# Kernel tuning notes

Measured on AMD Instinct MI355X. Metric: run time of the kernel, lower is better.

The kernel has to match this reference:

```python
import jax, jax.numpy as jnp
import numpy as np

NUM_HEADS = 8
HEAD_DIM = 64  # embed_dim 512 / 8 heads


def setup_inputs() -> dict:
    key = jax.random.key(0)
    k1, k2, k3 = jax.random.split(key, 3)
    B, S, D = 2, 4096, 512
    # xavier-uniform-ish scales for faithfulness to init (values don't affect math)
    x = jax.random.normal(k1, (B, S, D), dtype=jnp.float32)
    qkv_w = jax.random.normal(k2, (3 * D, D), dtype=jnp.float32) * (1.0 / np.sqrt(D))
    qkv_b = jnp.zeros((3 * D,), dtype=jnp.float32)
    o_w = jax.random.normal(k3, (D, D), dtype=jnp.float32) * (1.0 / np.sqrt(D))
    o_b = jnp.zeros((D,), dtype=jnp.float32)
    return {"x": x, "qkv_w": qkv_w, "qkv_b": qkv_b, "o_w": o_w, "o_b": o_b}


def reference(x, qkv_w, qkv_b, o_w, o_b):
    B, S, D = x.shape
    H, hd = NUM_HEADS, HEAD_DIM
    # qkv projection: torch Linear is x @ W^T + b
    qkv = jnp.einsum('bsd,ed->bse', x, qkv_w) + qkv_b        # [B, S, 3D]
    qkv = qkv.reshape(B, S, H, 3 * hd).transpose(0, 2, 1, 3)  # [B, H, S, 3hd]
    q, k, v = jnp.split(qkv, 3, axis=-1)                      # each [B, H, S, hd]
    scale = 1.0 / jnp.sqrt(jnp.float32(hd))
    logits = jnp.einsum('bhqd,bhkd->bhqk', q, k) * scale      # [B, H, S, S]
    attn = jax.nn.softmax(logits, axis=-1)
    vals = jnp.einsum('bhqk,bhkd->bhqd', attn, v)             # [B, H, S, hd]
    vals = vals.transpose(0, 2, 1, 3).reshape(B, S, D)        # [B, S, D]
    o = jnp.einsum('bsd,ed->bse', vals, o_w) + o_b            # [B, S, D]
    return o
```

## Files before the change

### kernel.cpp

```cpp
#include <hip/hip_runtime.h>
#include <hip/hip_bf16.h>


typedef __attribute__((ext_vector_type(8)))  __bf16 bf16x8;
typedef __attribute__((ext_vector_type(2)))  __bf16 bf16x2;
typedef __attribute__((ext_vector_type(4))) float  f32x4;
typedef __attribute__((ext_vector_type(16))) float  f32x16;

__device__ __forceinline__ unsigned cvtpk(float a, float b) {
    bf16x2 t; t.x = (__bf16)a; t.y = (__bf16)b;
    union { bf16x2 v; unsigned u; } u; u.v = t; return u.u;
}
#if __has_builtin(__builtin_amdgcn_exp2f)
__device__ __forceinline__ float fexp2(float x) { return __builtin_amdgcn_exp2f(x); }
#else
__device__ __forceinline__ float fexp2(float x) { return exp2f(x); }
#endif
__device__ __forceinline__ void gload16(const unsigned short* g, unsigned short* l) {
    __builtin_amdgcn_global_load_lds(
        (const __attribute__((address_space(1))) void*)g,
        (__attribute__((address_space(3))) void*)l, 16, 0, 0);
}

__device__ __forceinline__ int swz(int row, int col) {
    return row * 64 + (col ^ ((row & 7) << 3));
}

__global__ __launch_bounds__(256) void qkv_qk_gemm(
    const float* __restrict__ X, const float* __restrict__ W,
    const float* __restrict__ bias,
    unsigned short* __restrict__ Qb, unsigned short* __restrict__ Kb)
{
    __shared__ __attribute__((aligned(16))) unsigned short SH[128 * 144];
    unsigned short* As = &SH[0];
    unsigned short* Bs = &SH[8192];
    const int tid = threadIdx.x;
    const int wid = tid >> 6, lane = tid & 63;
    const int hi = lane >> 4, lo = lane & 15;
    const int wm = wid >> 1, wn = wid & 1;
    const int m0 = blockIdx.x * 128;
    const int by3 = blockIdx.y & 3, tt = blockIdx.y >> 2;
    const float QSCL = 0.125f * 1.44269504088896f;
    const float sc = (tt == 0) ? QSCL : 1.0f;

    f32x4 acc[4][4] = {};

    for (int k0 = 0; k0 < 512; k0 += 64) {
        __syncthreads();
        #pragma unroll
        for (int i = 0; i < 8; ++i) {
            const int c = i * 256 + tid;
            const int row = c >> 4, kc = (c & 15) << 2;
            const float4 va = *(const float4*)(X + (size_t)(m0 + row) * 512 + k0 + kc);
            uint2 pa; pa.x = cvtpk(va.x, va.y); pa.y = cvtpk(va.z, va.w);
            *(uint2*)&As[swz(row, kc)] = pa;
            const int nW = (by3 * 2 + (row >> 6)) * 192 + tt * 64 + (row & 63);
            const float4 vb = *(const float4*)(W + (size_t)nW * 512 + k0 + kc);
            uint2 pb; pb.x = cvtpk(vb.x, vb.y); pb.y = cvtpk(vb.z, vb.w);
            *(uint2*)&Bs[swz(row, kc)] = pb;
        }
        __syncthreads();
        #pragma unroll
        for (int ks = 0; ks < 2; ++ks) {
            bf16x8 af[4], bfr[4];
            #pragma unroll
            for (int mi = 0; mi < 4; ++mi)
                af[mi] = *(const bf16x8*)&As[swz(wm * 64 + mi * 16 + lo, ks * 32 + hi * 8)];
            #pragma unroll
            for (int ni = 0; ni < 4; ++ni)
                bfr[ni] = *(const bf16x8*)&Bs[swz(wn * 64 + ni * 16 + lo, ks * 32 + hi * 8)];
            #pragma unroll
            for (int mi = 0; mi < 4; ++mi)
                #pragma unroll
                for (int ni = 0; ni < 4; ++ni)
                    acc[mi][ni] = __builtin_amdgcn_mfma_f32_16x16x32_bf16(
                        bfr[ni], af[mi], acc[mi][ni], 0, 0, 0);
        }
    }
    __syncthreads();

    {
        #pragma unroll
        for (int ni = 0; ni < 4; ++ni) {
            const int hq = by3 * 2 + wn;
            const float4 bv4 = *(const float4*)&bias[hq * 192 + tt * 64 + ni * 16 + hi * 4];
            #pragma unroll
            for (int mi = 0; mi < 4; ++mi) {
                const int srow_ = wm * 64 + mi * 16 + lo;
                uint2 w;
                w.x = cvtpk((acc[mi][ni][0] + bv4.x) * sc, (acc[mi][ni][1] + bv4.y) * sc);
                w.y = cvtpk((acc[mi][ni][2] + bv4.z) * sc, (acc[mi][ni][3] + bv4.w) * sc);
                *(uint2*)&SH[srow_ * 144 + wn * 72 + ni * 16 + hi * 4] = w;
            }
        }
    }
    __syncthreads();

    const int b = m0 >> 12, sb = m0 & 4095;
    unsigned short* dst = tt ? Kb : Qb;
    #pragma unroll
    for (int c = 0; c < 2; ++c) {
        const int h = by3 * 2 + c;
        #pragma unroll
        for (int qq = 0; qq < 4; ++qq) {
            const int slot = qq * 256 + tid;
            const int row = slot >> 3, g = slot & 7;
            const uint4 v = *(const uint4*)&SH[row * 144 + c * 72 + g * 8];
            *(uint4*)(dst + (((size_t)(b * 8 + h)) * 4096 + sb + row) * 64 + g * 8) = v;
        }
    }
}

__global__ __launch_bounds__(256) void qkv_v_gemm(
    const float* __restrict__ X, const float* __restrict__ W,
    const float* __restrict__ bias, unsigned short* __restrict__ Vtg)
{
    __shared__ __attribute__((aligned(16))) unsigned short SH[128 * 144];
    unsigned short* As = &SH[0];
    unsigned short* Bs = &SH[8192];
    const int tid = threadIdx.x;
    const int wid = tid >> 6, lane = tid & 63;
    const int hi = lane >> 4, lo = lane & 15;
    const int wm = wid >> 1, wn = wid & 1;
    const int m0 = blockIdx.x * 128;
    const int by = blockIdx.y;

    f32x4 acc[4][4] = {};

    for (int k0 = 0; k0 < 512; k0 += 64) {
        __syncthreads();
        #pragma unroll
        for (int i = 0; i < 8; ++i) {
            const int c = i * 256 + tid;
            const int row = c >> 4, kc = (c & 15) << 2;
            const float4 va = *(const float4*)(X + (size_t)(m0 + row) * 512 + k0 + kc);
            uint2 pa; pa.x = cvtpk(va.x, va.y); pa.y = cvtpk(va.z, va.w);
            *(uint2*)&As[swz(row, kc)] = pa;
            const int nW = (by * 2 + (row >> 6)) * 192 + 128 + (row & 63);
            const float4 vb = *(const float4*)(W + (size_t)nW * 512 + k0 + kc);
            uint2 pb; pb.x = cvtpk(vb.x, vb.y); pb.y = cvtpk(vb.z, vb.w);
            *(uint2*)&Bs[swz(row, kc)] = pb;
        }
        __syncthreads();
        #pragma unroll
        for (int ks = 0; ks < 2; ++ks) {
            bf16x8 af[4], bfr[4];
            #pragma unroll
            for (int mi = 0; mi < 4; ++mi)
                af[mi] = *(const bf16x8*)&As[swz(wm * 64 + mi * 16 + lo, ks * 32 + hi * 8)];
            #pragma unroll
            for (int ni = 0; ni < 4; ++ni)
                bfr[ni] = *(const bf16x8*)&Bs[swz(wn * 64 + ni * 16 + lo, ks * 32 + hi * 8)];
            #pragma unroll
            for (int mi = 0; mi < 4; ++mi)
                #pragma unroll
                for (int ni = 0; ni < 4; ++ni)
                    acc[mi][ni] = __builtin_amdgcn_mfma_f32_16x16x32_bf16(
                        af[mi], bfr[ni], acc[mi][ni], 0, 0, 0);
        }
    }
    __syncthreads();

    #pragma unroll
    for (int ni = 0; ni < 4; ++ni) {
        const int d = ni * 16 + lo;
        const float bv = bias[(by * 2 + wn) * 192 + 128 + d];
        #pragma unroll
        for (int mi = 0; mi < 4; ++mi) {
            const int ml = wm * 64 + mi * 16 + hi * 4;
            uint2 w;
            w.x = cvtpk(acc[mi][ni][0] + bv, acc[mi][ni][1] + bv);
            w.y = cvtpk(acc[mi][ni][2] + bv, acc[mi][ni][3] + bv);
            *(uint2*)&SH[wn * 8704 + d * 136 + ml] = w;
        }
    }
    __syncthreads();

    const int b = m0 >> 12, sb = m0 & 4095;
    #pragma unroll
    for (int qq = 0; qq < 8; ++qq) {
        const int slot = qq * 256 + tid;
        const int c = slot >> 10, d = (slot >> 4) & 63, mb = slot & 15;
        const int src = c * 8704 + d * 136 + 16 * (mb >> 1) + 4 * (mb & 1);
        const uint2 a  = *(const uint2*)&SH[src];
        const uint2 bb = *(const uint2*)&SH[src + 8];
        uint4 w; w.x = a.x; w.y = a.y; w.z = bb.x; w.w = bb.y;
        const int h = by * 2 + c;
        *(uint4*)(Vtg + ((size_t)((b * 8 + h) * 64 + d)) * 4096 + sb + 8 * mb) = w;
    }
}

__global__ __launch_bounds__(512, 2) void attn_fwd(
    const unsigned short* __restrict__ Qb,
    const unsigned short* __restrict__ Kb,
    const unsigned short* __restrict__ Vtg,
    unsigned short* __restrict__ Ob)
{
    __shared__ __attribute__((aligned(16))) unsigned short smem[2][4][2][4096];

    const int tid = threadIdx.x;
    const int wid = tid >> 6, lane = tid & 63;
    const int l31 = lane & 31, hl = lane >> 5;
    const int n_ = blockIdx.x;
    const int bh = (n_ & 7) * 2 + ((n_ >> 3) & 1);
    const int qb = n_ >> 4;
    const int b = bh >> 3, h = bh & 7;
    const int q0 = qb * 256 + wid * 32;
    const size_t kbase = (size_t)bh * 4096 * 64;
    const size_t vbase = (size_t)bh * 64 * 4096;

    const int srow = tid >> 3;
    const int sg = (tid & 7) ^ (srow & 7);
    const unsigned short* kS = Kb + kbase + (size_t)srow * 64 + sg * 8;
    const unsigned short* vS = Vtg + vbase + (size_t)srow * 4096 + sg * 8;

    bf16x8 qf[4];
    #pragma unroll
    for (int dk = 0; dk < 4; ++dk)
        qf[dk] = *(const bf16x8*)(Qb + kbase + (size_t)(q0 + l31) * 64 + dk * 16 + hl * 8);

    f32x16 o0 = {}, o1 = {};
    float l_run = 0.0f;

    const int s7 = l31 & 7;
    const int baseA = l31 * 64, baseB = (32 + l31) * 64;
    const int ldst = tid * 8;

    #pragma unroll
    for (int i = 0; i < 4; ++i) {
        gload16(kS + (size_t)i * 4096, &smem[0][i][0][ldst]);
        gload16(vS + (size_t)i * 64,   &smem[0][i][1][ldst]);
    }
    asm volatile("s_waitcnt vmcnt(0)" ::: "memory");
    __builtin_amdgcn_s_barrier();
    __builtin_amdgcn_sched_barrier(0);

    for (int g = 0; g < 16; ++g) {
        const int cur = g & 1;
        if (g < 15) {
            #pragma unroll
            for (int i = 0; i < 4; ++i) {
                const size_t T = 4 * (g + 1) + i;
                gload16(kS + T * 4096, &smem[cur ^ 1][i][0][ldst]);
                gload16(vS + T * 64,   &smem[cur ^ 1][i][1][ldst]);
            }
        }
        #pragma unroll
        for (int ti = 0; ti < 4; ++ti) {
            const unsigned short* KT = &smem[cur][ti][0][0];
            const unsigned short* VT = &smem[cur][ti][1][0];

            f32x16 s0 = {}, s1 = {};
            __builtin_amdgcn_s_setprio(1);
            #pragma unroll
            for (int dk = 0; dk < 4; ++dk) {
                const int gk = dk * 2 + hl;
                const bf16x8 kA = *(const bf16x8*)(KT + baseA + 8 * (gk ^ s7));
                const bf16x8 kB = *(const bf16x8*)(KT + baseB + 8 * (gk ^ s7));
                s0 = __builtin_amdgcn_mfma_f32_32x32x16_bf16(kA, qf[dk], s0, 0, 0, 0);
                s1 = __builtin_amdgcn_mfma_f32_32x32x16_bf16(kB, qf[dk], s1, 0, 0, 0);
            }
            __builtin_amdgcn_s_setprio(0);

            #pragma unroll
            for (int i = 0; i < 16; ++i) {
                s0[i] = fexp2(s0[i]);
                s1[i] = fexp2(s1[i]);
            }
            float lsA = 0.f, lsB = 0.f, lsC = 0.f, lsD = 0.f;
            #pragma unroll
            for (int i = 0; i < 4; ++i) {
                lsA += s0[i];      lsB += s0[i + 4];
                lsA += s0[i + 8];  lsB += s0[i + 12];
                lsC += s1[i];      lsD += s1[i + 4];
                lsC += s1[i + 8];  lsD += s1[i + 12];
            }
            l_run += (lsA + lsB) + (lsC + lsD);

            union U8 { unsigned u[4]; bf16x8 v; };
            U8 p0, p1, p2, p3;
            #pragma unroll
            for (int i = 0; i < 4; ++i) {
                p0.u[i] = cvtpk(s0[2 * i],     s0[2 * i + 1]);
                p1.u[i] = cvtpk(s0[2 * i + 8], s0[2 * i + 9]);
                p2.u[i] = cvtpk(s1[2 * i],     s1[2 * i + 1]);
                p3.u[i] = cvtpk(s1[2 * i + 8], s1[2 * i + 9]);
            }
            const bf16x8 pf[4] = { p0.v, p1.v, p2.v, p3.v };

            __builtin_amdgcn_s_setprio(1);
            #pragma unroll
            for (int ks = 0; ks < 4; ++ks) {
                const int gv = ((2 * ks + hl) ^ s7) << 3;
                const bf16x8 va = *(const bf16x8*)(VT + baseA + gv);
                const bf16x8 vb = *(const bf16x8*)(VT + baseB + gv);
                o0 = __builtin_amdgcn_mfma_f32_32x32x16_bf16(va, pf[ks], o0, 0, 0, 0);
                o1 = __builtin_amdgcn_mfma_f32_32x32x16_bf16(vb, pf[ks], o1, 0, 0, 0);
            }
            __builtin_amdgcn_s_setprio(0);
        }
        asm volatile("s_waitcnt vmcnt(0)" ::: "memory");
        __builtin_amdgcn_s_barrier();
        __builtin_amdgcn_sched_barrier(0);
    }

    l_run += __shfl_xor(l_run, 32);
    unsigned short* Ew = &smem[0][0][0][0] + wid * 2048;
    const int prow = l31 * 64;
    const float inv = 1.0f / l_run;
    #pragma unroll
    for (int u = 0; u < 4; ++u) {
        uint2 w0, w1;
        w0.x = cvtpk(o0[4 * u] * inv, o0[4 * u + 1] * inv);
        w0.y = cvtpk(o0[4 * u + 2] * inv, o0[4 * u + 3] * inv);
        *(uint2*)&Ew[prow + ((u ^ s7) << 3) + (hl << 2)] = w0;
        w1.x = cvtpk(o1[4 * u] * inv, o1[4 * u + 1] * inv);
        w1.y = cvtpk(o1[4 * u + 2] * inv, o1[4 * u + 3] * inv);
        *(uint2*)&Ew[prow + (((4 + u) ^ s7) << 3) + (hl << 2)] = w1;
    }
    asm volatile("s_waitcnt lgkmcnt(0)" ::: "memory");
    __builtin_amdgcn_sched_barrier(0);
    #pragma unroll
    for (int rr = 0; rr < 4; ++rr) {
        const int qrow = (lane >> 3) + rr * 8;
        const int gphys = (lane & 7) ^ (qrow & 7);
        const uint4 v = *(const uint4*)&Ew[qrow * 64 + gphys * 8];
        *(uint4*)(Ob + ((size_t)b * 4096 + q0 + qrow) * 512 + h * 64 + (lane & 7) * 8) = v;
    }
}

__global__ __launch_bounds__(256) void oproj_gemm(
    const unsigned short* __restrict__ A, const float* __restrict__ W,
    const float* __restrict__ bias, float* __restrict__ C)
{
    __shared__ __attribute__((aligned(16))) unsigned short As[128 * 64];
    __shared__ __attribute__((aligned(16))) unsigned short Bs[128 * 64];
    const int tid = threadIdx.x;
    const int wid = tid >> 6, lane = tid & 63;
    const int hi = lane >> 4, lo = lane & 15;
    const int wm = wid >> 1, wn = wid & 1;
    const int m0 = blockIdx.x * 128, n0 = blockIdx.y * 128;

    f32x4 acc[4][4] = {};
    for (int k0 = 0; k0 < 512; k0 += 64) {
        __syncthreads();
        #pragma unroll
        for (int i = 0; i < 4; ++i) {
            const int c = i * 256 + tid;
            const int row = c >> 3, kc = (c & 7) << 3;
            *(uint4*)&As[swz(row, kc)] =
                *(const uint4*)(A + (size_t)(m0 + row) * 512 + k0 + kc);
        }
        #pragma unroll
        for (int i = 0; i < 8; ++i) {
            const int c = i * 256 + tid;
            const int row = c >> 4, kc = (c & 15) << 2;
            const float4 vb = *(const float4*)(W + (size_t)(n0 + row) * 512 + k0 + kc);
            uint2 pb; pb.x = cvtpk(vb.x, vb.y); pb.y = cvtpk(vb.z, vb.w);
            *(uint2*)&Bs[swz(row, kc)] = pb;
        }
        __syncthreads();
        #pragma unroll
        for (int ks = 0; ks < 2; ++ks) {
            bf16x8 af[4], bfr[4];
            #pragma unroll
            for (int mi = 0; mi < 4; ++mi)
                af[mi] = *(const bf16x8*)&As[swz(wm * 64 + mi * 16 + lo, ks * 32 + hi * 8)];
            #pragma unroll
            for (int ni = 0; ni < 4; ++ni)
                bfr[ni] = *(const bf16x8*)&Bs[swz(wn * 64 + ni * 16 + lo, ks * 32 + hi * 8)];
            #pragma unroll
            for (int mi = 0; mi < 4; ++mi)
                #pragma unroll
                for (int ni = 0; ni < 4; ++ni)
                    acc[mi][ni] = __builtin_amdgcn_mfma_f32_16x16x32_bf16(
                        af[mi], bfr[ni], acc[mi][ni], 0, 0, 0);
        }
    }

    #pragma unroll
    for (int mi = 0; mi < 4; ++mi) {
        #pragma unroll
        for (int ni = 0; ni < 4; ++ni) {
            const int n = n0 + wn * 64 + ni * 16 + lo;
            const float bv = bias[n];
            #pragma unroll
            for (int j = 0; j < 4; ++j) {
                const int m = m0 + wm * 64 + mi * 16 + hi * 4 + j;
                C[(size_t)m * 512 + n] = acc[mi][ni][j] + bv;
            }
        }
    }
}

extern "C" void kernel_launch(void* const* d_in, const int* in_sizes, int n_in,
                              void* d_out, int out_size, void* d_ws, size_t ws_size,
                              hipStream_t stream) {
    const float* x     = (const float*)d_in[0];
    const float* qkv_w = (const float*)d_in[1];
    const float* qkv_b = (const float*)d_in[2];
    const float* o_w   = (const float*)d_in[3];
    const float* o_b   = (const float*)d_in[4];
    float* out = (float*)d_out;

    const size_t NELEM = (size_t)2 * 8 * 4096 * 64;
    unsigned short* Qb  = (unsigned short*)d_ws;
    unsigned short* Kb  = Qb + NELEM;
    unsigned short* Vtg = Kb + NELEM;
    unsigned short* Ob  = Vtg + NELEM;

    qkv_qk_gemm<<<dim3(64, 8), 256, 0, stream>>>(x, qkv_w, qkv_b, Qb, Kb);
    qkv_v_gemm<<<dim3(64, 4), 256, 0, stream>>>(x, qkv_w, qkv_b, Vtg);
    attn_fwd<<<dim3(256), 512, 0, stream>>>(Qb, Kb, Vtg, Ob);
    oproj_gemm<<<dim3(64, 4), 256, 0, stream>>>(Ob, o_w, o_b, out);
}
```

Baseline: 124.2 us.

## Merge QK and V projection kernels; vectorize row-sum and unroll attention loop

The separate Q/K and V projection GEMMs become one launch with a 64x12 grid, where blocks with y>=8 take the V path. This removes a kernel launch and lets all projection blocks run in one wave. In the attention kernel, the softmax row-sum moves after the PV MFMAs and is accumulated with packed 2-wide float adds. The main loop also gets `#pragma unroll 2`. The unroll and the reordering may raise register pressure.

```diff
diff --git a/kernel.cpp b/kernel.cpp
--- a/kernel.cpp
+++ b/kernel.cpp
@@ -4,6 +4,7 @@
 
 typedef __attribute__((ext_vector_type(8)))  __bf16 bf16x8;
 typedef __attribute__((ext_vector_type(2)))  __bf16 bf16x2;
+typedef __attribute__((ext_vector_type(2))) float  f32x2;
 typedef __attribute__((ext_vector_type(4))) float  f32x4;
 typedef __attribute__((ext_vector_type(16))) float  f32x16;
 
@@ -26,10 +27,11 @@
     return row * 64 + (col ^ ((row & 7) << 3));
 }
 
-__global__ __launch_bounds__(256) void qkv_qk_gemm(
+__global__ __launch_bounds__(256) void qkv_gemm(
     const float* __restrict__ X, const float* __restrict__ W,
     const float* __restrict__ bias,
-    unsigned short* __restrict__ Qb, unsigned short* __restrict__ Kb)
+    unsigned short* __restrict__ Qb, unsigned short* __restrict__ Kb,
+    unsigned short* __restrict__ Vtg)
 {
     __shared__ __attribute__((aligned(16))) unsigned short SH[128 * 144];
     unsigned short* As = &SH[0];
@@ -39,47 +41,50 @@
     const int hi = lane >> 4, lo = lane & 15;
     const int wm = wid >> 1, wn = wid & 1;
     const int m0 = blockIdx.x * 128;
-    const int by3 = blockIdx.y & 3, tt = blockIdx.y >> 2;
-    const float QSCL = 0.125f * 1.44269504088896f;
-    const float sc = (tt == 0) ? QSCL : 1.0f;
+    const bool isV = (blockIdx.y >= 8);
+    const int b = m0 >> 12, sb = m0 & 4095;
 
     f32x4 acc[4][4] = {};
 
-    for (int k0 = 0; k0 < 512; k0 += 64) {
-        __syncthreads();
-        #pragma unroll
-        for (int i = 0; i < 8; ++i) {
-            const int c = i * 256 + tid;
-            const int row = c >> 4, kc = (c & 15) << 2;
-            const float4 va = *(const float4*)(X + (size_t)(m0 + row) * 512 + k0 + kc);
-            uint2 pa; pa.x = cvtpk(va.x, va.y); pa.y = cvtpk(va.z, va.w);
-            *(uint2*)&As[swz(row, kc)] = pa;
-            const int nW = (by3 * 2 + (row >> 6)) * 192 + tt * 64 + (row & 63);
-            const float4 vb = *(const float4*)(W + (size_t)nW * 512 + k0 + kc);
-            uint2 pb; pb.x = cvtpk(vb.x, vb.y); pb.y = cvtpk(vb.z, vb.w);
-            *(uint2*)&Bs[swz(row, kc)] = pb;
-        }
-        __syncthreads();
-        #pragma unroll
-        for (int ks = 0; ks < 2; ++ks) {
-            bf16x8 af[4], bfr[4];
-            #pragma unroll
-            for (int mi = 0; mi < 4; ++mi)
-                af[mi] = *(const bf16x8*)&As[swz(wm * 64 + mi * 16 + lo, ks * 32 + hi * 8)];
-            #pragma unroll
-            for (int ni = 0; ni < 4; ++ni)
-                bfr[ni] = *(const bf16x8*)&Bs[swz(wn * 64 + ni * 16 + lo, ks * 32 + hi * 8)];
-            #pragma unroll
-            for (int mi = 0; mi < 4; ++mi)
+    if (!isV) {
+        const int by3 = blockIdx.y & 3, tt = blockIdx.y >> 2;
+        const float QSCL = 0.125f * 1.44269504088896f;
+        const float sc = (tt == 0) ? QSCL : 1.0f;
+
+        for (int k0 = 0; k0 < 512; k0 += 64) {
+            __syncthreads();
+            #pragma unroll
+            for (int i = 0; i < 8; ++i) {
+                const int c = i * 256 + tid;
+                const int row = c >> 4, kc = (c & 15) << 2;
+                const float4 va = *(const float4*)(X + (size_t)(m0 + row) * 512 + k0 + kc);
+                uint2 pa; pa.x = cvtpk(va.x, va.y); pa.y = cvtpk(va.z, va.w);
+                *(uint2*)&As[swz(row, kc)] = pa;
+                const int nW = (by3 * 2 + (row >> 6)) * 192 + tt * 64 + (row & 63);
+                const float4 vb = *(const float4*)(W + (size_t)nW * 512 + k0 + kc);
+                uint2 pb; pb.x = cvtpk(vb.x, vb.y); pb.y = cvtpk(vb.z, vb.w);
+                *(uint2*)&Bs[swz(row, kc)] = pb;
+            }
+            __syncthreads();
+            #pragma unroll
+            for (int ks = 0; ks < 2; ++ks) {
+                bf16x8 af[4], bfr[4];
+                #pragma unroll
+                for (int mi = 0; mi < 4; ++mi)
+                    af[mi] = *(const bf16x8*)&As[swz(wm * 64 + mi * 16 + lo, ks * 32 + hi * 8)];
                 #pragma unroll
                 for (int ni = 0; ni < 4; ++ni)
-                    acc[mi][ni] = __builtin_amdgcn_mfma_f32_16x16x32_bf16(
-                        bfr[ni], af[mi], acc[mi][ni], 0, 0, 0);
-        }
-    }
-    __syncthreads();
-
-    {
+                    bfr[ni] = *(const bf16x8*)&Bs[swz(wn * 64 + ni * 16 + lo, ks * 32 + hi * 8)];
+                #pragma unroll
+                for (int mi = 0; mi < 4; ++mi)
+                    #pragma unroll
+                    for (int ni = 0; ni < 4; ++ni)
+                        acc[mi][ni] = __builtin_amdgcn_mfma_f32_16x16x32_bf16(
+                            bfr[ni], af[mi], acc[mi][ni], 0, 0, 0);
+            }
+        }
+        __syncthreads();
+
         #pragma unroll
         for (int ni = 0; ni < 4; ++ni) {
             const int hq = by3 * 2 + wn;
@@ -93,100 +98,83 @@
                 *(uint2*)&SH[srow_ * 144 + wn * 72 + ni * 16 + hi * 4] = w;
             }
         }
-    }
-    __syncthreads();
-
-    const int b = m0 >> 12, sb = m0 & 4095;
-    unsigned short* dst = tt ? Kb : Qb;
-    #pragma unroll
-    for (int c = 0; c < 2; ++c) {
-        const int h = by3 * 2 + c;
-        #pragma unroll
-        for (int qq = 0; qq < 4; ++qq) {
+        __syncthreads();
+
+        unsigned short* dst = tt ? Kb : Qb;
+        #pragma unroll
+        for (int c = 0; c < 2; ++c) {
+            const int h = by3 * 2 + c;
+            #pragma unroll
+            for (int qq = 0; qq < 4; ++qq) {
+                const int slot = qq * 256 + tid;
+                const int row = slot >> 3, g = slot & 7;
+                const uint4 v = *(const uint4*)&SH[row * 144 + c * 72 + g * 8];
+                *(uint4*)(dst + (((size_t)(b * 8 + h)) * 4096 + sb + row) * 64 + g * 8) = v;
+            }
+        }
+    } else {
+        const int by = blockIdx.y - 8;
+
+        for (int k0 = 0; k0 < 512; k0 += 64) {
+            __syncthreads();
+            #pragma unroll
+            for (int i = 0; i < 8; ++i) {
+                const int c = i * 256 + tid;
+                const int row = c >> 4, kc = (c & 15) << 2;
+                const float4 va = *(const float4*)(X + (size_t)(m0 + row) * 512 + k0 + kc);
+                uint2 pa; pa.x = cvtpk(va.x, va.y); pa.y = cvtpk(va.z, va.w);
+                *(uint2*)&As[swz(row, kc)] = pa;
+                const int nW = (by * 2 + (row >> 6)) * 192 + 128 + (row & 63);
+                const float4 vb = *(const float4*)(W + (size_t)nW * 512 + k0 + kc);
+                uint2 pb; pb.x = cvtpk(vb.x, vb.y); pb.y = cvtpk(vb.z, vb.w);
+                *(uint2*)&Bs[swz(row, kc)] = pb;
+            }
+            __syncthreads();
+            #pragma unroll
+            for (int ks = 0; ks < 2; ++ks) {
+                bf16x8 af[4], bfr[4];
+                #pragma unroll
+                for (int mi = 0; mi < 4; ++mi)
+                    af[mi] = *(const bf16x8*)&As[swz(wm * 64 + mi * 16 + lo, ks * 32 + hi * 8)];
+                #pragma unroll
+                for (int ni = 0; ni < 4; ++ni)
+                    bfr[ni] = *(const bf16x8*)&Bs[swz(wn * 64 + ni * 16 + lo, ks * 32 + hi * 8)];
+                #pragma unroll
+                for (int mi = 0; mi < 4; ++mi)
+                    #pragma unroll
+                    for (int ni = 0; ni < 4; ++ni)
+                        acc[mi][ni] = __builtin_amdgcn_mfma_f32_16x16x32_bf16(
+                            af[mi], bfr[ni], acc[mi][ni], 0, 0, 0);
+            }
+        }
+        __syncthreads();
+
+        #pragma unroll
+        for (int ni = 0; ni < 4; ++ni) {
+            const int d = ni * 16 + lo;
+            const float bv = bias[(by * 2 + wn) * 192 + 128 + d];
+            #pragma unroll
+            for (int mi = 0; mi < 4; ++mi) {
+                const int ml = wm * 64 + mi * 16 + hi * 4;
+                uint2 w;
+                w.x = cvtpk(acc[mi][ni][0] + bv, acc[mi][ni][1] + bv);
+                w.y = cvtpk(acc[mi][ni][2] + bv, acc[mi][ni][3] + bv);
+                *(uint2*)&SH[wn * 8704 + d * 136 + ml] = w;
+            }
+        }
+        __syncthreads();
+
+        #pragma unroll
+        for (int qq = 0; qq < 8; ++qq) {
             const int slot = qq * 256 + tid;
-            const int row = slot >> 3, g = slot & 7;
-            const uint4 v = *(const uint4*)&SH[row * 144 + c * 72 + g * 8];
-            *(uint4*)(dst + (((size_t)(b * 8 + h)) * 4096 + sb + row) * 64 + g * 8) = v;
-        }
-    }
-}
-
-__global__ __launch_bounds__(256) void qkv_v_gemm(
-    const float* __restrict__ X, const float* __restrict__ W,
-    const float* __restrict__ bias, unsigned short* __restrict__ Vtg)
-{
-    __shared__ __attribute__((aligned(16))) unsigned short SH[128 * 144];
-    unsigned short* As = &SH[0];
-    unsigned short* Bs = &SH[8192];
-    const int tid = threadIdx.x;
-    const int wid = tid >> 6, lane = tid & 63;
-    const int hi = lane >> 4, lo = lane & 15;
-    const int wm = wid >> 1, wn = wid & 1;
-    const int m0 = blockIdx.x * 128;
-    const int by = blockIdx.y;
-
-    f32x4 acc[4][4] = {};
-
-    for (int k0 = 0; k0 < 512; k0 += 64) {
-        __syncthreads();
-        #pragma unroll
-        for (int i = 0; i < 8; ++i) {
-            const int c = i * 256 + tid;
-            const int row = c >> 4, kc = (c & 15) << 2;
-            const float4 va = *(const float4*)(X + (size_t)(m0 + row) * 512 + k0 + kc);
-            uint2 pa; pa.x = cvtpk(va.x, va.y); pa.y = cvtpk(va.z, va.w);
-            *(uint2*)&As[swz(row, kc)] = pa;
-            const int nW = (by * 2 + (row >> 6)) * 192 + 128 + (row & 63);
-            const float4 vb = *(const float4*)(W + (size_t)nW * 512 + k0 + kc);
-            uint2 pb; pb.x = cvtpk(vb.x, vb.y); pb.y = cvtpk(vb.z, vb.w);
-            *(uint2*)&Bs[swz(row, kc)] = pb;
-        }
-        __syncthreads();
-        #pragma unroll
-        for (int ks = 0; ks < 2; ++ks) {
-            bf16x8 af[4], bfr[4];
-            #pragma unroll
-            for (int mi = 0; mi < 4; ++mi)
-                af[mi] = *(const bf16x8*)&As[swz(wm * 64 + mi * 16 + lo, ks * 32 + hi * 8)];
-            #pragma unroll
-            for (int ni = 0; ni < 4; ++ni)
-                bfr[ni] = *(const bf16x8*)&Bs[swz(wn * 64 + ni * 16 + lo, ks * 32 + hi * 8)];
-            #pragma unroll
-            for (int mi = 0; mi < 4; ++mi)
-                #pragma unroll
-                for (int ni = 0; ni < 4; ++ni)
-                    acc[mi][ni] = __builtin_amdgcn_mfma_f32_16x16x32_bf16(
-                        af[mi], bfr[ni], acc[mi][ni], 0, 0, 0);
-        }
-    }
-    __syncthreads();
-
-    #pragma unroll
-    for (int ni = 0; ni < 4; ++ni) {
-        const int d = ni * 16 + lo;
-        const float bv = bias[(by * 2 + wn) * 192 + 128 + d];
-        #pragma unroll
-        for (int mi = 0; mi < 4; ++mi) {
-            const int ml = wm * 64 + mi * 16 + hi * 4;
-            uint2 w;
-            w.x = cvtpk(acc[mi][ni][0] + bv, acc[mi][ni][1] + bv);
-            w.y = cvtpk(acc[mi][ni][2] + bv, acc[mi][ni][3] + bv);
-            *(uint2*)&SH[wn * 8704 + d * 136 + ml] = w;
-        }
-    }
-    __syncthreads();
-
-    const int b = m0 >> 12, sb = m0 & 4095;
-    #pragma unroll
-    for (int qq = 0; qq < 8; ++qq) {
-        const int slot = qq * 256 + tid;
-        const int c = slot >> 10, d = (slot >> 4) & 63, mb = slot & 15;
-        const int src = c * 8704 + d * 136 + 16 * (mb >> 1) + 4 * (mb & 1);
-        const uint2 a  = *(const uint2*)&SH[src];
-        const uint2 bb = *(const uint2*)&SH[src + 8];
-        uint4 w; w.x = a.x; w.y = a.y; w.z = bb.x; w.w = bb.y;
-        const int h = by * 2 + c;
-        *(uint4*)(Vtg + ((size_t)((b * 8 + h) * 64 + d)) * 4096 + sb + 8 * mb) = w;
+            const int c = slot >> 10, d = (slot >> 4) & 63, mb = slot & 15;
+            const int src = c * 8704 + d * 136 + 16 * (mb >> 1) + 4 * (mb & 1);
+            const uint2 a  = *(const uint2*)&SH[src];
+            const uint2 bb = *(const uint2*)&SH[src + 8];
+            uint4 w; w.x = a.x; w.y = a.y; w.z = bb.x; w.w = bb.y;
+            const int h = by * 2 + c;
+            *(uint4*)(Vtg + ((size_t)((b * 8 + h) * 64 + d)) * 4096 + sb + 8 * mb) = w;
+        }
     }
 }
 
@@ -220,7 +208,7 @@
         qf[dk] = *(const bf16x8*)(Qb + kbase + (size_t)(q0 + l31) * 64 + dk * 16 + hl * 8);
 
     f32x16 o0 = {}, o1 = {};
-    float l_run = 0.0f;
+    f32x2 l2 = {0.f, 0.f};
 
     const int s7 = l31 & 7;
     const int baseA = l31 * 64, baseB = (32 + l31) * 64;
@@ -235,6 +223,7 @@
     __builtin_amdgcn_s_barrier();
     __builtin_amdgcn_sched_barrier(0);
 
+    #pragma unroll 2
     for (int g = 0; g < 16; ++g) {
         const int cur = g & 1;
         if (g < 15) {
@@ -267,15 +256,6 @@
                 s0[i] = fexp2(s0[i]);
                 s1[i] = fexp2(s1[i]);
             }
-            float lsA = 0.f, lsB = 0.f, lsC = 0.f, lsD = 0.f;
-            #pragma unroll
-            for (int i = 0; i < 4; ++i) {
-                lsA += s0[i];      lsB += s0[i + 4];
-                lsA += s0[i + 8];  lsB += s0[i + 12];
-                lsC += s1[i];      lsD += s1[i + 4];
-                lsC += s1[i + 8];  lsD += s1[i + 12];
-            }
-            l_run += (lsA + lsB) + (lsC + lsD);
 
             union U8 { unsigned u[4]; bf16x8 v; };
             U8 p0, p1, p2, p3;
@@ -298,12 +278,20 @@
                 o1 = __builtin_amdgcn_mfma_f32_32x32x16_bf16(vb, pf[ks], o1, 0, 0, 0);
             }
             __builtin_amdgcn_s_setprio(0);
+
+            f32x2 a2 = {s0[0], s0[1]};
+            #pragma unroll
+            for (int i = 1; i < 8; ++i) { f32x2 t = {s0[2 * i], s0[2 * i + 1]}; a2 += t; }
+            #pragma unroll
+            for (int i = 0; i < 8; ++i) { f32x2 t = {s1[2 * i], s1[2 * i + 1]}; a2 += t; }
+            l2 += a2;
         }
         asm volatile("s_waitcnt vmcnt(0)" ::: "memory");
         __builtin_amdgcn_s_barrier();
         __builtin_amdgcn_sched_barrier(0);
     }
 
+    float l_run = l2.x + l2.y;
     l_run += __shfl_xor(l_run, 32);
     unsigned short* Ew = &smem[0][0][0][0] + wid * 2048;
     const int prow = l31 * 64;
@@ -409,8 +397,7 @@
     unsigned short* Vtg = Kb + NELEM;
     unsigned short* Ob  = Vtg + NELEM;
 
-    qkv_qk_gemm<<<dim3(64, 8), 256, 0, stream>>>(x, qkv_w, qkv_b, Qb, Kb);
-    qkv_v_gemm<<<dim3(64, 4), 256, 0, stream>>>(x, qkv_w, qkv_b, Vtg);
+    qkv_gemm<<<dim3(64, 12), 256, 0, stream>>>(x, qkv_w, qkv_b, Qb, Kb, Vtg);
     attn_fwd<<<dim3(256), 512, 0, stream>>>(Qb, Kb, Vtg, Ob);
     oproj_gemm<<<dim3(64, 4), 256, 0, stream>>>(Ob, o_w, o_b, out);
 }
```

Result: slower. 127.1 us (+2.4%).
